# Kernel optimization log

Hardware: AMD Instinct MI355X
Metric: run time of the kernel (lower is better)

## Reference

```python
import jax, jax.numpy as jnp
import numpy as np

GROUP = 64

def dequant(W_q, scale, zero):
    # W_q: [out, in] int, scale/zero: [out, in//GROUP]
    out, din = W_q.shape
    g = din // GROUP
    Wq = W_q.reshape(out, g, GROUP).astype(scale.dtype)
    W = (Wq - zero[:, :, None]) * scale[:, :, None]
    return W.reshape(out, din)

def setup_inputs() -> dict:
    key = jax.random.key(0)
    ks = jax.random.split(key, 10)
    T, H, F = 512, 4096, 14336
    return {
        "hidden_states": jax.random.normal(ks[0], (T, H), jnp.float32),
        "W1_q": jax.random.randint(ks[1], (F, H), 0, 16, jnp.int32),
        "w1_scale": jax.random.uniform(ks[2], (F, H // GROUP), jnp.float32, 1e-3, 0.02),
        "w1_zero": jax.random.uniform(ks[3], (F, H // GROUP), jnp.float32, 6.0, 9.0),
        "W3_q": jax.random.randint(ks[4], (F, H), 0, 16, jnp.int32),
        "w3_scale": jax.random.uniform(ks[5], (F, H // GROUP), jnp.float32, 1e-3, 0.02),
        "w3_zero": jax.random.uniform(ks[6], (F, H // GROUP), jnp.float32, 6.0, 9.0),
        "W2_q": jax.random.randint(ks[7], (H, F), 0, 16, jnp.int32),
        "w2_scale": jax.random.uniform(ks[8], (H, F // GROUP), jnp.float32, 1e-3, 0.02),
        "w2_zero": jax.random.uniform(ks[9], (H, F // GROUP), jnp.float32, 6.0, 9.0),
    }

def reference(hidden_states, W1_q, w1_scale, w1_zero, W3_q, w3_scale, w3_zero, W2_q, w2_scale, w2_zero):
    W1 = dequant(W1_q, w1_scale, w1_zero)  # [F, H]
    W3 = dequant(W3_q, w3_scale, w3_zero)  # [F, H]
    W2 = dequant(W2_q, w2_scale, w2_zero)  # [H, F]
    g = jax.nn.silu(hidden_states @ W1.T) * (hidden_states @ W3.T)  # [T, F]
    return g @ W2.T  # [T, H]
```

## Files before the change

### kernel.cpp

```cpp
#include <hip/hip_runtime.h>
#include <hip/hip_bf16.h>

#define T_DIM 512
#define H_DIM 4096
#define F_DIM 14336
#define KSEG  8

typedef __attribute__((ext_vector_type(8))) short bf16x8;
typedef __attribute__((ext_vector_type(4))) float f32x4;

__device__ __forceinline__ unsigned short f2bf(float f) {
    union { float f; unsigned u; } v; v.f = f;
    unsigned r = v.u + 0x7fffu + ((v.u >> 16) & 1u);
    return (unsigned short)(r >> 16);
}

__device__ __forceinline__ void barrier_lgkm() {
    __asm__ __volatile__("" ::: "memory");
    __builtin_amdgcn_s_waitcnt(0xC07F);
    __builtin_amdgcn_s_barrier();
    __asm__ __volatile__("" ::: "memory");
}

__global__ __launch_bounds__(256) void zero_out(float4* __restrict__ out) {
    out[blockIdx.x * 256 + threadIdx.x] = make_float4(0.f, 0.f, 0.f, 0.f);
}

__global__ __launch_bounds__(256) void cvt_x(const float* __restrict__ X,
                                             unsigned short* __restrict__ Xb) {
    int i = (blockIdx.x * 256 + threadIdx.x) * 4;
    float4 v = *(const float4*)&X[i];
    ushort4 o;
    o.x = f2bf(v.x); o.y = f2bf(v.y); o.z = f2bf(v.z); o.w = f2bf(v.w);
    *(ushort4*)&Xb[i] = o;
}

__global__ __launch_bounds__(256, 2)
void gate_up_kernel(const unsigned short* __restrict__ Xb,
                    const int* __restrict__ W1q, const float* __restrict__ sc1,
                    const float* __restrict__ zp1,
                    const int* __restrict__ W3q, const float* __restrict__ sc3,
                    const float* __restrict__ zp3,
                    unsigned short* __restrict__ G)
{
    constexpr int LK = 72;
    __shared__ __align__(16) char smem[(128 + 64 + 64) * LK * 2];
    unsigned short* sX  = (unsigned short*)smem;
    unsigned short* sW1 = (unsigned short*)(smem + 128 * LK * 2);
    unsigned short* sW3 = (unsigned short*)(smem + 192 * LK * 2);
    float* sEx = (float*)smem;

    const int t = threadIdx.x, wave = t >> 6, lane = t & 63;
    const int r = lane & 15, q = lane >> 4;
    const int mh  = (wave & 1) * 64;
    const int mat = wave >> 1;

    const int b = blockIdx.x;
    const int xcd = b & 7, lb = b >> 3;
    const int m0 = (lb & 3) * 128;
    const int n0 = (xcd * 28 + (lb >> 2)) * 64;
    const int SG = H_DIM / 64;

    const int xrow = t >> 3, xch = (t & 7) * 8;
    const int wrow = t >> 4, wc = (t & 15) * 4;

    int4 pW1[4], pW3[4];
    #pragma unroll
    for (int i = 0; i < 4; ++i) {
        size_t off = (size_t)(n0 + wrow + 16 * i) * H_DIM + wc;
        pW1[i] = *(const int4*)&W1q[off];
        pW3[i] = *(const int4*)&W3q[off];
    }

    f32x4 acc[4][4];
    #pragma unroll
    for (int a = 0; a < 4; ++a)
        #pragma unroll
        for (int c = 0; c < 4; ++c) acc[a][c] = (f32x4){0.f, 0.f, 0.f, 0.f};

    for (int k0 = 0; k0 < H_DIM; k0 += 64) {
        const int gidx = k0 >> 6;

        #pragma unroll
        for (int i = 0; i < 4; ++i) {
            int4 xv = *(const int4*)&Xb[(size_t)(m0 + xrow + 32 * i) * H_DIM + k0 + xch];
            *(int4*)&sX[(xrow + 32 * i) * LK + xch] = xv;
        }
        #pragma unroll
        for (int i = 0; i < 4; ++i) {
            int row = wrow + 16 * i;
            int sidx = (n0 + row) * SG + gidx;
            float s = sc1[sidx], nzs = -zp1[sidx] * s;
            int4 qv = pW1[i];
            ushort4 o;
            o.x = f2bf(fmaf((float)qv.x, s, nzs)); o.y = f2bf(fmaf((float)qv.y, s, nzs));
            o.z = f2bf(fmaf((float)qv.z, s, nzs)); o.w = f2bf(fmaf((float)qv.w, s, nzs));
            *(ushort4*)&sW1[row * LK + wc] = o;
            s = sc3[sidx]; nzs = -zp3[sidx] * s;
            qv = pW3[i];
            o.x = f2bf(fmaf((float)qv.x, s, nzs)); o.y = f2bf(fmaf((float)qv.y, s, nzs));
            o.z = f2bf(fmaf((float)qv.z, s, nzs)); o.w = f2bf(fmaf((float)qv.w, s, nzs));
            *(ushort4*)&sW3[row * LK + wc] = o;
        }
        int kn = k0 + 64;
        if (kn < H_DIM) {
            #pragma unroll
            for (int i = 0; i < 4; ++i) {
                size_t off = (size_t)(n0 + wrow + 16 * i) * H_DIM + kn + wc;
                pW1[i] = *(const int4*)&W1q[off];
                pW3[i] = *(const int4*)&W3q[off];
            }
        }
        barrier_lgkm();

        const unsigned short* sB = mat ? sW3 : sW1;
        #pragma unroll
        for (int kh = 0; kh < 2; ++kh) {
            const int kb = kh * 32 + q * 8;
            bf16x8 av[4], bv[4];
            #pragma unroll
            for (int im = 0; im < 4; ++im)
                av[im] = *(const bf16x8*)&sX[(mh + im * 16 + r) * LK + kb];
            #pragma unroll
            for (int j = 0; j < 4; ++j)
                bv[j] = *(const bf16x8*)&sB[(j * 16 + r) * LK + kb];
            #pragma unroll
            for (int im = 0; im < 4; ++im)
                #pragma unroll
                for (int j = 0; j < 4; ++j)
                    acc[im][j] = __builtin_amdgcn_mfma_f32_16x16x32_bf16(av[im], bv[j], acc[im][j], 0, 0, 0);
        }
        barrier_lgkm();
    }

    if (mat == 1) {
        #pragma unroll
        for (int im = 0; im < 4; ++im)
            #pragma unroll
            for (int j = 0; j < 4; ++j)
                #pragma unroll
                for (int reg = 0; reg < 4; ++reg)
                    sEx[(mh + im * 16 + q * 4 + reg) * 65 + j * 16 + r] = acc[im][j][reg];
    }
    __syncthreads();
    if (mat == 0) {
        #pragma unroll
        for (int im = 0; im < 4; ++im)
            #pragma unroll
            for (int j = 0; j < 4; ++j)
                #pragma unroll
                for (int reg = 0; reg < 4; ++reg) {
                    int ml = mh + im * 16 + q * 4 + reg;
                    int nl = j * 16 + r;
                    float g1 = acc[im][j][reg];
                    float g3 = sEx[ml * 65 + nl];
                    float val = g1 / (1.f + __expf(-g1)) * g3;
                    G[(size_t)(m0 + ml) * F_DIM + n0 + nl] = f2bf(val);
                }
    }
}

__global__ __launch_bounds__(256, 2)
void down_kernel(const unsigned short* __restrict__ G,
                 const int* __restrict__ W2q, const float* __restrict__ sc2,
                 const float* __restrict__ zp2,
                 float* __restrict__ Out)
{
    constexpr int LK = 72;
    __shared__ __align__(16) char smem[(128 + 128) * LK * 2];
    unsigned short* sA = (unsigned short*)smem;
    unsigned short* sW = (unsigned short*)(smem + 128 * LK * 2);

    const int t = threadIdx.x, wave = t >> 6, lane = t & 63;
    const int r = lane & 15, q = lane >> 4;
    const int wm = (wave & 1) * 64, wn = (wave >> 1) * 64;

    const int b = blockIdx.x;
    const int xcd = b & 7, lb = b >> 3;
    const int m0 = (lb & 3) * 128;
    const int pair = xcd * 32 + (lb >> 2);
    const int n0 = (pair >> 3) * 128;
    const int kbeg = (pair & 7) * (F_DIM / KSEG);
    const int kend = kbeg + (F_DIM / KSEG);
    const int SG = F_DIM / 64;

    const int arow = t >> 3, ach = (t & 7) * 8;
    const int wrow = t >> 4, wc = (t & 15) * 4;

    int4 pW[8];
    #pragma unroll
    for (int i = 0; i < 8; ++i)
        pW[i] = *(const int4*)&W2q[(size_t)(n0 + wrow + 16 * i) * F_DIM + kbeg + wc];

    f32x4 acc[4][4];
    #pragma unroll
    for (int a = 0; a < 4; ++a)
        #pragma unroll
        for (int c = 0; c < 4; ++c) acc[a][c] = (f32x4){0.f, 0.f, 0.f, 0.f};

    for (int k0 = kbeg; k0 < kend; k0 += 64) {
        const int gidx = k0 >> 6;

        #pragma unroll
        for (int i = 0; i < 4; ++i) {
            int4 gv = *(const int4*)&G[(size_t)(m0 + arow + 32 * i) * F_DIM + k0 + ach];
            *(int4*)&sA[(arow + 32 * i) * LK + ach] = gv;
        }
        #pragma unroll
        for (int i = 0; i < 8; ++i) {
            int row = wrow + 16 * i;
            int sidx = (n0 + row) * SG + gidx;
            float s = sc2[sidx], nzs = -zp2[sidx] * s;
            int4 qv = pW[i];
            ushort4 o;
            o.x = f2bf(fmaf((float)qv.x, s, nzs)); o.y = f2bf(fmaf((float)qv.y, s, nzs));
            o.z = f2bf(fmaf((float)qv.z, s, nzs)); o.w = f2bf(fmaf((float)qv.w, s, nzs));
            *(ushort4*)&sW[row * LK + wc] = o;
        }
        int kn = k0 + 64;
        if (kn < kend) {
            #pragma unroll
            for (int i = 0; i < 8; ++i)
                pW[i] = *(const int4*)&W2q[(size_t)(n0 + wrow + 16 * i) * F_DIM + kn + wc];
        }
        barrier_lgkm();

        #pragma unroll
        for (int kh = 0; kh < 2; ++kh) {
            const int kb = kh * 32 + q * 8;
            bf16x8 av[4], bv[4];
            #pragma unroll
            for (int im = 0; im < 4; ++im)
                av[im] = *(const bf16x8*)&sA[(wm + im * 16 + r) * LK + kb];
            #pragma unroll
            for (int j = 0; j < 4; ++j)
                bv[j] = *(const bf16x8*)&sW[(wn + j * 16 + r) * LK + kb];
            #pragma unroll
            for (int im = 0; im < 4; ++im)
                #pragma unroll
                for (int j = 0; j < 4; ++j)
                    acc[im][j] = __builtin_amdgcn_mfma_f32_16x16x32_bf16(av[im], bv[j], acc[im][j], 0, 0, 0);
        }
        barrier_lgkm();
    }

    #pragma unroll
    for (int im = 0; im < 4; ++im)
        #pragma unroll
        for (int j = 0; j < 4; ++j)
            #pragma unroll
            for (int reg = 0; reg < 4; ++reg) {
                int m = m0 + wm + im * 16 + q * 4 + reg;
                int h = n0 + wn + j * 16 + r;
                atomicAdd(&Out[(size_t)m * H_DIM + h], acc[im][j][reg]);
            }
}

extern "C" void kernel_launch(void* const* d_in, const int* in_sizes, int n_in,
                              void* d_out, int out_size, void* d_ws, size_t ws_size,
                              hipStream_t stream) {
    const float* X   = (const float*)d_in[0];
    const int*   W1q = (const int*)d_in[1];
    const float* s1  = (const float*)d_in[2];
    const float* z1  = (const float*)d_in[3];
    const int*   W3q = (const int*)d_in[4];
    const float* s3  = (const float*)d_in[5];
    const float* z3  = (const float*)d_in[6];
    const int*   W2q = (const int*)d_in[7];
    const float* s2  = (const float*)d_in[8];
    const float* z2  = (const float*)d_in[9];
    float* Out = (float*)d_out;

    unsigned short* Xb = (unsigned short*)d_ws;
    unsigned short* G  = (unsigned short*)((char*)d_ws + (4 << 20));

    zero_out<<<2048, 256, 0, stream>>>((float4*)Out);
    cvt_x<<<2048, 256, 0, stream>>>(X, Xb);
    gate_up_kernel<<<896, 256, 0, stream>>>(Xb, W1q, s1, z1, W3q, s3, z3, G);
    down_kernel<<<1024, 256, 0, stream>>>(G, W2q, s2, z2, Out);
}
```

Measured before the change: 921.3 us.

## Double-buffer LDS tiles, switch to fp16 MFMA, halve down-proj split-K

Both GEMM kernels now double-buffer shared memory, so the next tile is dequantized and staged while MFMAs run on the current one, with one barrier per iteration instead of two. Activations and the weight dequant switch from bf16 with software rounding to fp16 via the packed cvt_pkrtz instruction, which cuts conversion ALU work. The down projection uses 4 K segments instead of 8, giving 512 blocks and fewer output atomics. The costs are doubled LDS per block, which may lower occupancy, fp16 range and precision risk, and less parallelism in the down kernel.

```diff
diff --git a/kernel.cpp b/kernel.cpp
--- a/kernel.cpp
+++ b/kernel.cpp
@@ -4,16 +4,11 @@
 #define T_DIM 512
 #define H_DIM 4096
 #define F_DIM 14336
-#define KSEG  8
-
-typedef __attribute__((ext_vector_type(8))) short bf16x8;
-typedef __attribute__((ext_vector_type(4))) float f32x4;
-
-__device__ __forceinline__ unsigned short f2bf(float f) {
-    union { float f; unsigned u; } v; v.f = f;
-    unsigned r = v.u + 0x7fffu + ((v.u >> 16) & 1u);
-    return (unsigned short)(r >> 16);
-}
+#define KSEG  4
+
+typedef __fp16 f16x8 __attribute__((ext_vector_type(8)));
+typedef __fp16 f16x2 __attribute__((ext_vector_type(2)));
+typedef float f32x4 __attribute__((ext_vector_type(4)));
 
 __device__ __forceinline__ void barrier_lgkm() {
     __asm__ __volatile__("" ::: "memory");
@@ -27,33 +22,38 @@
 }
 
 __global__ __launch_bounds__(256) void cvt_x(const float* __restrict__ X,
-                                             unsigned short* __restrict__ Xb) {
+                                             _Float16* __restrict__ Xh) {
     int i = (blockIdx.x * 256 + threadIdx.x) * 4;
     float4 v = *(const float4*)&X[i];
-    ushort4 o;
-    o.x = f2bf(v.x); o.y = f2bf(v.y); o.z = f2bf(v.z); o.w = f2bf(v.w);
-    *(ushort4*)&Xb[i] = o;
+    union { struct { f16x2 a, b; } p; uint2 u; } u;
+    u.p.a = __builtin_amdgcn_cvt_pkrtz(v.x, v.y);
+    u.p.b = __builtin_amdgcn_cvt_pkrtz(v.z, v.w);
+    *(uint2*)&Xh[i] = u.u;
+}
+
+__device__ __forceinline__ ushort4 dq4(int4 qv, float s, float nzs) {
+    union { struct { f16x2 lo, hi; } h; ushort4 u; } u;
+    u.h.lo = __builtin_amdgcn_cvt_pkrtz(fmaf((float)qv.x, s, nzs),
+                                        fmaf((float)qv.y, s, nzs));
+    u.h.hi = __builtin_amdgcn_cvt_pkrtz(fmaf((float)qv.z, s, nzs),
+                                        fmaf((float)qv.w, s, nzs));
+    return u.u;
 }
 
 __global__ __launch_bounds__(256, 2)
-void gate_up_kernel(const unsigned short* __restrict__ Xb,
+void gate_up_kernel(const _Float16* __restrict__ Xh,
                     const int* __restrict__ W1q, const float* __restrict__ sc1,
                     const float* __restrict__ zp1,
                     const int* __restrict__ W3q, const float* __restrict__ sc3,
                     const float* __restrict__ zp3,
-                    unsigned short* __restrict__ G)
+                    _Float16* __restrict__ G)
 {
     constexpr int LK = 72;
-    __shared__ __align__(16) char smem[(128 + 64 + 64) * LK * 2];
-    unsigned short* sX  = (unsigned short*)smem;
-    unsigned short* sW1 = (unsigned short*)(smem + 128 * LK * 2);
-    unsigned short* sW3 = (unsigned short*)(smem + 192 * LK * 2);
-    float* sEx = (float*)smem;
+    __shared__ __align__(16) unsigned short smem[2][256 * LK];
 
     const int t = threadIdx.x, wave = t >> 6, lane = t & 63;
     const int r = lane & 15, q = lane >> 4;
-    const int mh  = (wave & 1) * 64;
-    const int mat = wave >> 1;
+    const int mh = (wave & 1) * 64, mat = wave >> 1;
 
     const int b = blockIdx.x;
     const int xcd = b & 7, lb = b >> 3;
@@ -64,75 +64,78 @@
     const int xrow = t >> 3, xch = (t & 7) * 8;
     const int wrow = t >> 4, wc = (t & 15) * 4;
 
-    int4 pW1[4], pW3[4];
-    #pragma unroll
-    for (int i = 0; i < 4; ++i) {
-        size_t off = (size_t)(n0 + wrow + 16 * i) * H_DIM + wc;
-        pW1[i] = *(const int4*)&W1q[off];
-        pW3[i] = *(const int4*)&W3q[off];
-    }
-
-    f32x4 acc[4][4];
-    #pragma unroll
-    for (int a = 0; a < 4; ++a)
-        #pragma unroll
-        for (int c = 0; c < 4; ++c) acc[a][c] = (f32x4){0.f, 0.f, 0.f, 0.f};
-
-    for (int k0 = 0; k0 < H_DIM; k0 += 64) {
-        const int gidx = k0 >> 6;
-
+    int4 rX[4], rW1[4], rW3[4];
+
+    auto load_tile = [&](int k0) {
+        #pragma unroll
+        for (int i = 0; i < 4; ++i)
+            rX[i] = *(const int4*)&Xh[(size_t)(m0 + xrow + 32 * i) * H_DIM + k0 + xch];
         #pragma unroll
         for (int i = 0; i < 4; ++i) {
-            int4 xv = *(const int4*)&Xb[(size_t)(m0 + xrow + 32 * i) * H_DIM + k0 + xch];
-            *(int4*)&sX[(xrow + 32 * i) * LK + xch] = xv;
-        }
+            size_t off = (size_t)(n0 + wrow + 16 * i) * H_DIM + k0 + wc;
+            rW1[i] = *(const int4*)&W1q[off];
+            rW3[i] = *(const int4*)&W3q[off];
+        }
+    };
+    auto stage = [&](unsigned short* buf, int gidx) {
+        unsigned short* sX  = buf;
+        unsigned short* sW1 = buf + 128 * LK;
+        unsigned short* sW3 = buf + 192 * LK;
+        #pragma unroll
+        for (int i = 0; i < 4; ++i)
+            *(int4*)&sX[(xrow + 32 * i) * LK + xch] = rX[i];
         #pragma unroll
         for (int i = 0; i < 4; ++i) {
             int row = wrow + 16 * i;
             int sidx = (n0 + row) * SG + gidx;
             float s = sc1[sidx], nzs = -zp1[sidx] * s;
-            int4 qv = pW1[i];
-            ushort4 o;
-            o.x = f2bf(fmaf((float)qv.x, s, nzs)); o.y = f2bf(fmaf((float)qv.y, s, nzs));
-            o.z = f2bf(fmaf((float)qv.z, s, nzs)); o.w = f2bf(fmaf((float)qv.w, s, nzs));
-            *(ushort4*)&sW1[row * LK + wc] = o;
+            *(ushort4*)&sW1[row * LK + wc] = dq4(rW1[i], s, nzs);
             s = sc3[sidx]; nzs = -zp3[sidx] * s;
-            qv = pW3[i];
-            o.x = f2bf(fmaf((float)qv.x, s, nzs)); o.y = f2bf(fmaf((float)qv.y, s, nzs));
-            o.z = f2bf(fmaf((float)qv.z, s, nzs)); o.w = f2bf(fmaf((float)qv.w, s, nzs));
-            *(ushort4*)&sW3[row * LK + wc] = o;
-        }
-        int kn = k0 + 64;
-        if (kn < H_DIM) {
-            #pragma unroll
-            for (int i = 0; i < 4; ++i) {
-                size_t off = (size_t)(n0 + wrow + 16 * i) * H_DIM + kn + wc;
-                pW1[i] = *(const int4*)&W1q[off];
-                pW3[i] = *(const int4*)&W3q[off];
-            }
-        }
-        barrier_lgkm();
-
-        const unsigned short* sB = mat ? sW3 : sW1;
+            *(ushort4*)&sW3[row * LK + wc] = dq4(rW3[i], s, nzs);
+        }
+    };
+
+    f32x4 acc[4][4];
+    #pragma unroll
+    for (int a = 0; a < 4; ++a)
+        #pragma unroll
+        for (int c = 0; c < 4; ++c) acc[a][c] = (f32x4){0.f, 0.f, 0.f, 0.f};
+
+    load_tile(0);
+    stage(smem[0], 0);
+    load_tile(64);
+    barrier_lgkm();
+
+    int p = 0;
+    for (int k0 = 0; k0 < H_DIM; k0 += 64) {
+        const unsigned short* sX = smem[p];
+        const unsigned short* sB = smem[p] + (mat ? 192 * LK : 128 * LK);
         #pragma unroll
         for (int kh = 0; kh < 2; ++kh) {
             const int kb = kh * 32 + q * 8;
-            bf16x8 av[4], bv[4];
-            #pragma unroll
-            for (int im = 0; im < 4; ++im)
-                av[im] = *(const bf16x8*)&sX[(mh + im * 16 + r) * LK + kb];
-            #pragma unroll
-            for (int j = 0; j < 4; ++j)
-                bv[j] = *(const bf16x8*)&sB[(j * 16 + r) * LK + kb];
+            f16x8 av[4], bv[4];
+            #pragma unroll
+            for (int im = 0; im < 4; ++im)
+                av[im] = *(const f16x8*)&sX[(mh + im * 16 + r) * LK + kb];
+            #pragma unroll
+            for (int j = 0; j < 4; ++j)
+                bv[j] = *(const f16x8*)&sB[(j * 16 + r) * LK + kb];
             #pragma unroll
             for (int im = 0; im < 4; ++im)
                 #pragma unroll
                 for (int j = 0; j < 4; ++j)
-                    acc[im][j] = __builtin_amdgcn_mfma_f32_16x16x32_bf16(av[im], bv[j], acc[im][j], 0, 0, 0);
-        }
-        barrier_lgkm();
-    }
-
+                    acc[im][j] = __builtin_amdgcn_mfma_f32_16x16x32_f16(av[im], bv[j], acc[im][j], 0, 0, 0);
+        }
+        int k1 = k0 + 64;
+        if (k1 < H_DIM) {
+            stage(smem[p ^ 1], k1 >> 6);
+            if (k1 + 64 < H_DIM) load_tile(k1 + 64);
+            barrier_lgkm();
+        }
+        p ^= 1;
+    }
+
+    float* sEx = (float*)&smem[0][0];
     if (mat == 1) {
         #pragma unroll
         for (int im = 0; im < 4; ++im)
@@ -155,21 +158,19 @@
                     float g1 = acc[im][j][reg];
                     float g3 = sEx[ml * 65 + nl];
                     float val = g1 / (1.f + __expf(-g1)) * g3;
-                    G[(size_t)(m0 + ml) * F_DIM + n0 + nl] = f2bf(val);
+                    G[(size_t)(m0 + ml) * F_DIM + n0 + nl] = (_Float16)val;
                 }
     }
 }
 
 __global__ __launch_bounds__(256, 2)
-void down_kernel(const unsigned short* __restrict__ G,
+void down_kernel(const _Float16* __restrict__ G,
                  const int* __restrict__ W2q, const float* __restrict__ sc2,
                  const float* __restrict__ zp2,
                  float* __restrict__ Out)
 {
     constexpr int LK = 72;
-    __shared__ __align__(16) char smem[(128 + 128) * LK * 2];
-    unsigned short* sA = (unsigned short*)smem;
-    unsigned short* sW = (unsigned short*)(smem + 128 * LK * 2);
+    __shared__ __align__(16) unsigned short smem[2][256 * LK];
 
     const int t = threadIdx.x, wave = t >> 6, lane = t & 63;
     const int r = lane & 15, q = lane >> 4;
@@ -178,70 +179,78 @@
     const int b = blockIdx.x;
     const int xcd = b & 7, lb = b >> 3;
     const int m0 = (lb & 3) * 128;
-    const int pair = xcd * 32 + (lb >> 2);
-    const int n0 = (pair >> 3) * 128;
-    const int kbeg = (pair & 7) * (F_DIM / KSEG);
+    const int rest = lb >> 2;
+    const int n0 = (xcd * 4 + (rest & 3)) * 128;
+    const int kbeg = (rest >> 2) * (F_DIM / KSEG);
     const int kend = kbeg + (F_DIM / KSEG);
     const int SG = F_DIM / 64;
 
     const int arow = t >> 3, ach = (t & 7) * 8;
     const int wrow = t >> 4, wc = (t & 15) * 4;
 
-    int4 pW[8];
-    #pragma unroll
-    for (int i = 0; i < 8; ++i)
-        pW[i] = *(const int4*)&W2q[(size_t)(n0 + wrow + 16 * i) * F_DIM + kbeg + wc];
-
-    f32x4 acc[4][4];
-    #pragma unroll
-    for (int a = 0; a < 4; ++a)
-        #pragma unroll
-        for (int c = 0; c < 4; ++c) acc[a][c] = (f32x4){0.f, 0.f, 0.f, 0.f};
-
-    for (int k0 = kbeg; k0 < kend; k0 += 64) {
-        const int gidx = k0 >> 6;
-
-        #pragma unroll
-        for (int i = 0; i < 4; ++i) {
-            int4 gv = *(const int4*)&G[(size_t)(m0 + arow + 32 * i) * F_DIM + k0 + ach];
-            *(int4*)&sA[(arow + 32 * i) * LK + ach] = gv;
-        }
+    int4 rA[4], rW[8];
+
+    auto load_tile = [&](int k0) {
+        #pragma unroll
+        for (int i = 0; i < 4; ++i)
+            rA[i] = *(const int4*)&G[(size_t)(m0 + arow + 32 * i) * F_DIM + k0 + ach];
+        #pragma unroll
+        for (int i = 0; i < 8; ++i)
+            rW[i] = *(const int4*)&W2q[(size_t)(n0 + wrow + 16 * i) * F_DIM + k0 + wc];
+    };
+    auto stage = [&](unsigned short* buf, int gidx) {
+        unsigned short* sA = buf;
+        unsigned short* sW = buf + 128 * LK;
+        #pragma unroll
+        for (int i = 0; i < 4; ++i)
+            *(int4*)&sA[(arow + 32 * i) * LK + ach] = rA[i];
         #pragma unroll
         for (int i = 0; i < 8; ++i) {
             int row = wrow + 16 * i;
             int sidx = (n0 + row) * SG + gidx;
             float s = sc2[sidx], nzs = -zp2[sidx] * s;
-            int4 qv = pW[i];
-            ushort4 o;
-            o.x = f2bf(fmaf((float)qv.x, s, nzs)); o.y = f2bf(fmaf((float)qv.y, s, nzs));
-            o.z = f2bf(fmaf((float)qv.z, s, nzs)); o.w = f2bf(fmaf((float)qv.w, s, nzs));
-            *(ushort4*)&sW[row * LK + wc] = o;
-        }
-        int kn = k0 + 64;
-        if (kn < kend) {
-            #pragma unroll
-            for (int i = 0; i < 8; ++i)
-                pW[i] = *(const int4*)&W2q[(size_t)(n0 + wrow + 16 * i) * F_DIM + kn + wc];
-        }
-        barrier_lgkm();
-
+            *(ushort4*)&sW[row * LK + wc] = dq4(rW[i], s, nzs);
+        }
+    };
+
+    f32x4 acc[4][4];
+    #pragma unroll
+    for (int a = 0; a < 4; ++a)
+        #pragma unroll
+        for (int c = 0; c < 4; ++c) acc[a][c] = (f32x4){0.f, 0.f, 0.f, 0.f};
+
+    load_tile(kbeg);
+    stage(smem[0], kbeg >> 6);
+    load_tile(kbeg + 64);
+    barrier_lgkm();
+
+    int p = 0;
+    for (int k0 = kbeg; k0 < kend; k0 += 64) {
+        const unsigned short* sA = smem[p];
+        const unsigned short* sW = smem[p] + 128 * LK;
         #pragma unroll
         for (int kh = 0; kh < 2; ++kh) {
             const int kb = kh * 32 + q * 8;
-            bf16x8 av[4], bv[4];
-            #pragma unroll
-            for (int im = 0; im < 4; ++im)
-                av[im] = *(const bf16x8*)&sA[(wm + im * 16 + r) * LK + kb];
-            #pragma unroll
-            for (int j = 0; j < 4; ++j)
-                bv[j] = *(const bf16x8*)&sW[(wn + j * 16 + r) * LK + kb];
+            f16x8 av[4], bv[4];
+            #pragma unroll
+            for (int im = 0; im < 4; ++im)
+                av[im] = *(const f16x8*)&sA[(wm + im * 16 + r) * LK + kb];
+            #pragma unroll
+            for (int j = 0; j < 4; ++j)
+                bv[j] = *(const f16x8*)&sW[(wn + j * 16 + r) * LK + kb];
             #pragma unroll
             for (int im = 0; im < 4; ++im)
                 #pragma unroll
                 for (int j = 0; j < 4; ++j)
-                    acc[im][j] = __builtin_amdgcn_mfma_f32_16x16x32_bf16(av[im], bv[j], acc[im][j], 0, 0, 0);
-        }
-        barrier_lgkm();
+                    acc[im][j] = __builtin_amdgcn_mfma_f32_16x16x32_f16(av[im], bv[j], acc[im][j], 0, 0, 0);
+        }
+        int k1 = k0 + 64;
+        if (k1 < kend) {
+            stage(smem[p ^ 1], k1 >> 6);
+            if (k1 + 64 < kend) load_tile(k1 + 64);
+            barrier_lgkm();
+        }
+        p ^= 1;
     }
 
     #pragma unroll
@@ -271,11 +280,11 @@
     const float* z2  = (const float*)d_in[9];
     float* Out = (float*)d_out;
 
-    unsigned short* Xb = (unsigned short*)d_ws;
-    unsigned short* G  = (unsigned short*)((char*)d_ws + (4 << 20));
+    _Float16* Xh = (_Float16*)d_ws;
+    _Float16* G  = (_Float16*)((char*)d_ws + (4 << 20));
 
     zero_out<<<2048, 256, 0, stream>>>((float4*)Out);
-    cvt_x<<<2048, 256, 0, stream>>>(X, Xb);
-    gate_up_kernel<<<896, 256, 0, stream>>>(Xb, W1q, s1, z1, W3q, s3, z3, G);
-    down_kernel<<<1024, 256, 0, stream>>>(G, W2q, s2, z2, Out);
-}
+    cvt_x<<<2048, 256, 0, stream>>>(X, Xh);
+    gate_up_kernel<<<896, 256, 0, stream>>>(Xh, W1q, s1, z1, W3q, s3, z3, G);
+    down_kernel<<<512, 256, 0, stream>>>(G, W2q, s2, z2, Out);
+}
```

Result: slower. 1.197 ms (+29.9%).
